# Kernel optimization log

Measured on AMD Instinct MI355X. Metric: run time of the kernel, lower is better.

The kernel has to match this reference:

```python
import jax, jax.numpy as jnp
import numpy as np

ANGLE_SCALE = 100.0
DIST_SCALE = 100.0
DIST_BOUNDARY = 0.0
HID = 128
N_HIDDEN = 2  # output_layer
EPS = 1e-08


def _mlp(x, w0, b0, ws, bs):
    # Linear, then N_HIDDEN x (ReLU, Linear)
    h = x @ w0 + b0
    for i in range(ws.shape[0]):
        h = jax.nn.relu(h) @ ws[i] + bs[i]
    return h


def _capsule_endpoints(x):
    # x: [..., 9] -> A, B endpoints of capsule segment, radius r
    c, s = jnp.cos(x[..., 3:4] * ANGLE_SCALE), jnp.sin(x[..., 3:4] * ANGLE_SCALE)
    half = x[..., 2:3] / 2
    ctr = x[..., 0:2]
    off = jnp.concatenate([half * c, half * s], axis=-1)
    return ctr - off, ctr + off, x[..., 4:5]


def _pt_seg_dist(P, A, AB, AB_sq):
    t = jnp.clip(((P - A) * AB).sum(-1, keepdims=True) / AB_sq, 0.0, 1.0)
    Q = A + t * AB
    return jnp.linalg.norm(P - Q, axis=-1, keepdims=True)


def _dist_to_capsule(init_e, query_e):
    A1, B1, r1 = _capsule_endpoints(init_e)
    A2, B2, r2 = _capsule_endpoints(query_e)
    A1B1, A2B2 = B1 - A1, B2 - A2
    s1 = (A1B1 ** 2).sum(-1, keepdims=True) + EPS
    s2 = (A2B2 ** 2).sum(-1, keepdims=True) + EPS
    d = jnp.minimum(
        jnp.minimum(_pt_seg_dist(A2, A1, A1B1, s1), _pt_seg_dist(B2, A1, A1B1, s1)),
        jnp.minimum(_pt_seg_dist(A1, A2, A2B2, s2), _pt_seg_dist(B1, A2, A2B2, s2)),
    )
    return d - r1 - r2


def setup_inputs() -> dict:
    key = jax.random.key(0)
    ks = jax.random.split(key, 32)
    B, O, T = 64, 64, 64
    f = lambda k, shp, scale=1.0: jax.random.normal(k, shp, dtype=jnp.float32) * scale
    inp = {
        'init_x': f(ks[0], (B, O, 9)),
        'query_x': f(ks[1], (B, T, 9)),
        'init_v': f(ks[2], (B, O, 2)),
        'query_v': f(ks[3], (B, T, 2)),
        'init_angular_v': f(ks[4], (B, O, 1)),
        'query_angular_v': f(ks[5], (B, T, 1)),
        'trunk_w0': f(ks[6], (9, HID), 0.3), 'trunk_b0': f(ks[7], (HID,), 0.1),
        'trunk_ws': f(ks[8], (N_HIDDEN, HID, HID), 0.08), 'trunk_bs': f(ks[9], (N_HIDDEN, HID), 0.1),
        'branch_w0': f(ks[10], (5, HID), 0.3), 'branch_b0': f(ks[11], (HID,), 0.1),
        'branch_ws': f(ks[12], (N_HIDDEN, HID, HID), 0.08), 'branch_bs': f(ks[13], (N_HIDDEN, HID), 0.1),
        'out_w': f(ks[14], (HID, 3), 0.08), 'out_b': f(ks[15], (3,), 0.1),
        'spring_w0': f(ks[16], (1, HID), 0.3), 'spring_b0': f(ks[17], (HID,), 0.1),
        'spring_w1': f(ks[18], (HID, 1), 0.08), 'spring_b1': f(ks[19], (1,), 0.1),
        'joint_w0': f(ks[20], (15, HID), 0.3), 'joint_b0': f(ks[21], (HID,), 0.1),
        'joint_w1': f(ks[22], (HID, 2), 0.08), 'joint_b1': f(ks[23], (2,), 0.1),
    }
    return inp


def reference(init_x, query_x, init_v, query_v, init_angular_v, query_angular_v,
              trunk_w0, trunk_b0, trunk_ws, trunk_bs,
              branch_w0, branch_b0, branch_ws, branch_bs,
              out_w, out_b, spring_w0, spring_b0, spring_w1, spring_b1,
              joint_w0, joint_b0, joint_w1, joint_b1):
    B, O, _ = init_x.shape
    T = query_x.shape[1]
    # pairwise broadcast: init along obj axis (dim1), query along target axis (dim2)
    init_e = jnp.broadcast_to(init_x[:, :, None, :], (B, O, T, 9))
    query_e = jnp.broadcast_to(query_x[:, None, :, :], (B, O, T, 9))
    rel = query_e[..., :2] - init_e[..., :2]
    query_e = jnp.concatenate([rel, query_e[..., 2:]], axis=-1)
    init_e = jnp.concatenate([jnp.zeros_like(rel), init_e[..., 2:]], axis=-1)
    qv = query_v[:, None, :, :] - init_v[:, :, None, :]           # [B,O,T,2]
    qav = query_angular_v[:, None, :, :] - init_angular_v[:, :, None, :]  # [B,O,T,1]
    iav = jnp.broadcast_to(init_angular_v[:, :, None, :], (B, O, T, 1))

    dist = _dist_to_capsule(init_e, query_e)
    dist_mask = (dist <= DIST_BOUNDARY).astype(jnp.float32)
    dist_input = dist * dist_mask * DIST_SCALE

    branch_in = init_e[..., :5]
    trunk_in = jnp.concatenate([query_e[..., :5], qv, qav, dist_input], axis=-1)
    branch_out = _mlp(branch_in, branch_w0, branch_b0, branch_ws, branch_bs)
    trunk_out = _mlp(trunk_in, trunk_w0, trunk_b0, trunk_ws, trunk_bs)
    force = (branch_out * trunk_out) @ out_w + out_b  # [B,O,T,3]

    # spring force
    have_spring = ((init_e[..., 8:9] == query_e[..., 8:9]) & (init_e[..., 8:9] > 0)).astype(jnp.float32)
    dvec = init_e[..., :2] - query_e[..., :2]
    length = jnp.linalg.norm(dvec, axis=-1, keepdims=True)
    dvec = dvec / (length + EPS)
    sf = jax.nn.relu(length @ spring_w0 + spring_b0) @ spring_w1 + spring_b1  # [B,O,T,1]
    sf = sf * dvec
    sf = jnp.concatenate([sf, jnp.zeros_like(sf[..., :1])], axis=-1) * have_spring

    # joint force (torch .long() truncates toward zero)
    i7, q7 = init_e[..., 7:8], query_e[..., 7:8]
    have_joint = ((jnp.trunc(i7) == jnp.trunc(q7)) & (i7 > 0)).astype(jnp.float32)
    joint_in = jnp.concatenate([init_e[..., :5], query_e[..., :5], qv, iav, qav, i7 - jnp.trunc(i7)], axis=-1)
    jf = jax.nn.relu(joint_in @ joint_w0 + joint_b0) @ joint_w1 + joint_b1  # [B,O,T,2]
    jf = jf * have_joint
    jf = jnp.concatenate([jf, jnp.zeros_like(jf[..., :1])], axis=-1)

    force = force * dist_mask + sf + jf
    return force
```

## Files before the change

kernel.cpp:

```cpp
#include <hip/hip_runtime.h>
#include <math.h>


typedef _Float16 h4v __attribute__((ext_vector_type(4)));
typedef _Float16 h8v __attribute__((ext_vector_type(8)));
typedef float    f4v __attribute__((ext_vector_type(4)));

#define AH 136

#define TW0_OFF 0
#define JW0_OFF 4096
#define TWS_OFF 8192
#define BW0_OFF 40960
#define BWS_OFF 45056
#define W_TOTAL 77824
#define BR_OFF_F (W_TOTAL/2)

#define H_ACTA 0
#define H_ACTB 8704
#define H_TINB 8704
#define H_JINB 10752
#define SMH_SIZE 17408

#define F_SCAL  0
#define SMF_SIZE 384

#define FRAG_BLOCKS 304
#define BR_BLOCKS   256

__global__ __launch_bounds__(256)
void prep_kernel(const float* __restrict__ tw0, const float* __restrict__ tws,
                 const float* __restrict__ jw0, const float* __restrict__ bw0,
                 const float* __restrict__ bws, const float* __restrict__ bb0,
                 const float* __restrict__ bbs, const float* __restrict__ init_x,
                 _Float16* __restrict__ wsH, float* __restrict__ brw)
{
    __shared__ float bsm[2*16*132];
    const int tid = threadIdx.x;

    if (blockIdx.x < FRAG_BLOCKS) {
        int idx = blockIdx.x * 256 + tid;
        if (idx >= W_TOTAL) return;
        const int j = idx & 7;
        const int lane = (idx >> 3) & 63;
        const int q = lane >> 4, r = lane & 15;
        _Float16 v;
        if (idx < JW0_OFF) {
            int mt = idx >> 9;
            int k = q*8 + j, m = mt*16 + r;
            v = (k < 9) ? (_Float16)tw0[k*128 + m] : (_Float16)0.f;
        } else if (idx < TWS_OFF) {
            int mt = (idx - JW0_OFF) >> 9;
            int k = q*8 + j, m = mt*16 + r;
            v = (k < 15) ? (_Float16)jw0[k*128 + m] : (_Float16)0.f;
        } else if (idx < BW0_OFF) {
            int e = idx - TWS_OFF;
            int ks = (e >> 9) & 3, mt = (e >> 11) & 7, l = e >> 14;
            int k = ks*32 + q*8 + j, m = mt*16 + r;
            v = (_Float16)tws[l*16384 + k*128 + m];
        } else if (idx < BWS_OFF) {
            int mt = (idx - BW0_OFF) >> 9;
            int k = q*8 + j, m = mt*16 + r;
            v = (k < 5) ? (_Float16)bw0[k*128 + m] : (_Float16)0.f;
        } else {
            int e = idx - BWS_OFF;
            int ks = (e >> 9) & 3, mt = (e >> 11) & 7, l = e >> 14;
            int k = ks*32 + q*8 + j, m = mt*16 + r;
            v = (_Float16)bws[l*16384 + k*128 + m];
        }
        wsH[idx] = v;
        return;
    }

    const int blk2 = blockIdx.x - FRAG_BLOCKS;
    const int row0 = blk2*16;
    const int lane = tid & 63, w = tid >> 6;
    const int q = lane >> 4, r = lane & 15;
    float* h0 = bsm;
    float* h1 = bsm + 16*132;

    for (int e = tid; e < 2048; e += 256) {
        const int rw = e >> 7, n = e & 127;
        const float* ixp = init_x + (row0 + rw)*9;
        float acc = bb0[n];
        acc = fmaf(ixp[2], bw0[2*128 + n], acc);
        acc = fmaf(ixp[3], bw0[3*128 + n], acc);
        acc = fmaf(ixp[4], bw0[4*128 + n], acc);
        h0[rw*132 + n] = acc;
    }
    __syncthreads();

    #pragma unroll
    for (int L = 0; L < 2; ++L) {
        const float* Wg = bws + L*16384;
        const float* bi = bbs + L*128;
        const float* in = (L == 0) ? h0 : h1;
        #pragma unroll
        for (int mi = 0; mi < 2; ++mi) {
            const int mt = w + mi*4;
            const int m0 = mt*16 + q*4;
            h8v af[4];
            #pragma unroll
            for (int ks = 0; ks < 4; ++ks)
                #pragma unroll
                for (int j = 0; j < 8; ++j)
                    af[ks][j] = (_Float16)Wg[(ks*32 + q*8 + j)*128 + mt*16 + r];
            f4v acc = *(const f4v*)&bi[m0];
            #pragma unroll
            for (int ks = 0; ks < 4; ++ks) {
                f4v x0 = *(const f4v*)&in[r*132 + ks*32 + q*8];
                f4v x1 = *(const f4v*)&in[r*132 + ks*32 + q*8 + 4];
                h8v bf;
                #pragma unroll
                for (int i = 0; i < 4; ++i) {
                    bf[i]   = (_Float16)fmaxf(x0[i], 0.f);
                    bf[4+i] = (_Float16)fmaxf(x1[i], 0.f);
                }
                acc = __builtin_amdgcn_mfma_f32_16x16x32_f16(af[ks], bf, acc, 0, 0, 0);
            }
            if (L == 0)
                *(f4v*)&h1[r*132 + m0] = acc;
            else
                *(f4v*)&brw[(row0 + r)*128 + m0] = acc;
        }
        __syncthreads();
    }
}

__device__ __forceinline__ void layerK32_rw(const h8v af[2],
        const float* __restrict__ bias, const _Float16* __restrict__ inB,
        _Float16* __restrict__ actOut, int lane, int w)
{
    const int q = lane >> 4, r = lane & 15;
    #pragma unroll
    for (int nt = 0; nt < 4; ++nt) {
        h8v bf = *(const h8v*)&inB[(nt*64 + lane)*8];
        #pragma unroll
        for (int mi = 0; mi < 2; ++mi) {
            f4v acc = *(const f4v*)&bias[(2*w + mi)*16 + q*4];
            acc = __builtin_amdgcn_mfma_f32_16x16x32_f16(af[mi], bf, acc, 0, 0, 0);
            h4v o;
            #pragma unroll
            for (int i = 0; i < 4; ++i) o[i] = (_Float16)fmaxf(acc[i], 0.f);
            *(h4v*)&actOut[(nt*16 + r)*AH + (2*w + mi)*16 + q*4] = o;
        }
    }
}

__device__ __forceinline__ void layerK128_rw(const h8v af[2][4],
        const float* __restrict__ bias, const _Float16* __restrict__ actIn,
        _Float16* __restrict__ actOut, int lane, int w)
{
    const int q = lane >> 4, r = lane & 15;
    #pragma unroll
    for (int nt = 0; nt < 4; ++nt) {
        h8v bf[4];
        #pragma unroll
        for (int ks = 0; ks < 4; ++ks)
            bf[ks] = *(const h8v*)&actIn[(nt*16 + r)*AH + ks*32 + q*8];
        #pragma unroll
        for (int mi = 0; mi < 2; ++mi) {
            f4v acc = *(const f4v*)&bias[(2*w + mi)*16 + q*4];
            #pragma unroll
            for (int ks = 0; ks < 4; ++ks)
                acc = __builtin_amdgcn_mfma_f32_16x16x32_f16(af[mi][ks], bf[ks], acc, 0, 0, 0);
            h4v o;
            #pragma unroll
            for (int i = 0; i < 4; ++i) o[i] = (_Float16)fmaxf(acc[i], 0.f);
            *(h4v*)&actOut[(nt*16 + r)*AH + (2*w + mi)*16 + q*4] = o;
        }
    }
}

__device__ __forceinline__ void layerK128_regs_rw(const h8v af[2][4],
        const float* __restrict__ bias, const _Float16* __restrict__ actIn,
        f4v accT[2][4], int lane, int w)
{
    const int q = lane >> 4, r = lane & 15;
    #pragma unroll
    for (int nt = 0; nt < 4; ++nt) {
        h8v bf[4];
        #pragma unroll
        for (int ks = 0; ks < 4; ++ks)
            bf[ks] = *(const h8v*)&actIn[(nt*16 + r)*AH + ks*32 + q*8];
        #pragma unroll
        for (int mi = 0; mi < 2; ++mi) {
            f4v acc = *(const f4v*)&bias[(2*w + mi)*16 + q*4];
            #pragma unroll
            for (int ks = 0; ks < 4; ++ks)
                acc = __builtin_amdgcn_mfma_f32_16x16x32_f16(af[mi][ks], bf[ks], acc, 0, 0, 0);
            accT[mi][nt] = acc;
        }
    }
}

__global__ __launch_bounds__(256, 3)
void ff_kernel(const float* __restrict__ init_x,  const float* __restrict__ query_x,
               const float* __restrict__ init_v,  const float* __restrict__ query_v,
               const float* __restrict__ init_av, const float* __restrict__ query_av,
               const float* __restrict__ tb0, const float* __restrict__ tbs,
               const float* __restrict__ out_w, const float* __restrict__ out_b,
               const float* __restrict__ sw0, const float* __restrict__ sb0,
               const float* __restrict__ sw1, const float* __restrict__ sb1,
               const float* __restrict__ jb0,
               const float* __restrict__ jw1, const float* __restrict__ jb1,
               const _Float16* __restrict__ wsH, const float* __restrict__ brw,
               float* __restrict__ out)
{
    __shared__ __align__(16) _Float16 smh[SMH_SIZE];
    __shared__ float smf[SMF_SIZE];
    float* const fred = (float*)smh;
    const int tid = threadIdx.x;
    const int bid = blockIdx.x;
    const int o  = bid & 63;
    const int b  = bid >> 6;
    const int lane = tid & 63, w = tid >> 6;
    const int q = lane >> 4, r = lane & 15;
    const float* ix = init_x + (b*64 + o)*9;

    h8v afT0[2], afJ0[2], afT1[2][4], afT2[2][4];
    f4v br[2];
    #pragma unroll
    for (int mi = 0; mi < 2; ++mi) {
        const int mtg = 2*w + mi;
        afT0[mi] = *(const h8v*)&wsH[TW0_OFF + (mtg*64 + lane)*8];
        afJ0[mi] = *(const h8v*)&wsH[JW0_OFF + (mtg*64 + lane)*8];
        #pragma unroll
        for (int ks = 0; ks < 4; ++ks) {
            afT1[mi][ks] = *(const h8v*)&wsH[TWS_OFF + ((mtg*4 + ks)*64 + lane)*8];
            afT2[mi][ks] = *(const h8v*)&wsH[TWS_OFF + 16384 + ((mtg*4 + ks)*64 + lane)*8];
        }
        br[mi] = *(const f4v*)&brw[bid*128 + mtg*16 + q*4];
    }

    {
        const int tq = w*16 + r;
        const float* qx = query_x + (b*64 + tq)*9;
        const float ix0 = ix[0], ix1 = ix[1], ix2 = ix[2], ix3 = ix[3], ix4 = ix[4];
        const float ix7 = ix[7], ix8 = ix[8];
        const float qx0 = qx[0], qx1 = qx[1], qx2 = qx[2], qx3 = qx[3], qx4 = qx[4];
        const float qx7 = qx[7], qx8 = qx[8];
        const float rel0 = qx0 - ix0, rel1 = qx1 - ix1;

        float s1v, c1v; sincosf(ix3 * 100.f, &s1v, &c1v);
        float s2v, c2v; sincosf(qx3 * 100.f, &s2v, &c2v);
        const float h1 = ix2 * 0.5f, h2 = qx2 * 0.5f;
        const float o1x = h1*c1v, o1y = h1*s1v;
        const float o2x = h2*c2v, o2y = h2*s2v;
        const float A1x = -o1x, A1y = -o1y;
        const float A2x = rel0 - o2x, A2y = rel1 - o2y;
        const float B2x = rel0 + o2x, B2y = rel1 + o2y;
        const float ab1x = 2.f*o1x, ab1y = 2.f*o1y;
        const float ab2x = 2.f*o2x, ab2y = 2.f*o2y;
        const float s1sq = ab1x*ab1x + ab1y*ab1y + 1e-8f;
        const float s2sq = ab2x*ab2x + ab2y*ab2y + 1e-8f;

        float Px, Py, Ax, Ay, ABx, ABy, ss;
        if (q < 2) {
            Ax = A1x; Ay = A1y; ABx = ab1x; ABy = ab1y; ss = s1sq;
            Px = (q == 0) ? A2x : B2x;  Py = (q == 0) ? A2y : B2y;
        } else {
            Ax = A2x; Ay = A2y; ABx = ab2x; ABy = ab2y; ss = s2sq;
            Px = (q == 2) ? A1x : o1x;  Py = (q == 2) ? A1y : o1y;
        }
        float t = ((Px - Ax)*ABx + (Py - Ay)*ABy) / ss;
        t = fminf(fmaxf(t, 0.f), 1.f);
        const float dx = Px - (Ax + t*ABx);
        const float dy = Py - (Ay + t*ABy);
        float dq = sqrtf(dx*dx + dy*dy);
        dq = fminf(dq, __shfl_xor(dq, 16));
        dq = fminf(dq, __shfl_xor(dq, 32));

        if (q == 0) {
            const float dist = dq - ix4 - qx4;
            const float mask = (dist <= 0.f) ? 1.f : 0.f;
            const float dinp = dist * mask * 100.f;
            const float qv0 = query_v[(b*64+tq)*2+0] - init_v[(b*64+o)*2+0];
            const float qv1 = query_v[(b*64+tq)*2+1] - init_v[(b*64+o)*2+1];
            const float iav = init_av[b*64+o];
            const float qav = query_av[b*64+tq] - iav;

            const int fb = w*512 + r*8;
            h8v t0, t1 = {}, z = {};
            t0[0]=(_Float16)rel0; t0[1]=(_Float16)rel1; t0[2]=(_Float16)qx2;
            t0[3]=(_Float16)qx3;  t0[4]=(_Float16)qx4;  t0[5]=(_Float16)qv0;
            t0[6]=(_Float16)qv1;  t0[7]=(_Float16)qav;
            t1[0]=(_Float16)dinp;
            *(h8v*)&smh[H_TINB + fb]       = t0;
            *(h8v*)&smh[H_TINB + fb + 128] = t1;
            *(h8v*)&smh[H_TINB + fb + 256] = z;
            *(h8v*)&smh[H_TINB + fb + 384] = z;
            h8v j0, j1 = {};
            j0[0]=(_Float16)0.f;  j0[1]=(_Float16)0.f;  j0[2]=(_Float16)ix2;
            j0[3]=(_Float16)ix3;  j0[4]=(_Float16)ix4;  j0[5]=(_Float16)rel0;
            j0[6]=(_Float16)rel1; j0[7]=(_Float16)qx2;
            j1[0]=(_Float16)qx3;  j1[1]=(_Float16)qx4;  j1[2]=(_Float16)qv0;
            j1[3]=(_Float16)qv1;  j1[4]=(_Float16)iav;  j1[5]=(_Float16)qav;
            j1[6]=(_Float16)(ix7 - truncf(ix7));
            *(h8v*)&smh[H_JINB + fb]       = j0;
            *(h8v*)&smh[H_JINB + fb + 128] = j1;
            *(h8v*)&smh[H_JINB + fb + 256] = z;
            *(h8v*)&smh[H_JINB + fb + 384] = z;

            const float len = sqrtf(rel0*rel0 + rel1*rel1);
            const float inv = 1.f / (len + 1e-8f);
            smf[F_SCAL +       tq] = mask;
            smf[F_SCAL +  64 + tq] = len;
            smf[F_SCAL + 128 + tq] = -rel0 * inv;
            smf[F_SCAL + 192 + tq] = -rel1 * inv;
            smf[F_SCAL + 256 + tq] = ((ix8 == qx8) && (ix8 > 0.f)) ? 1.f : 0.f;
            smf[F_SCAL + 320 + tq] = ((truncf(ix7) == truncf(qx7)) && (ix7 > 0.f)) ? 1.f : 0.f;
        }
    }
    __syncthreads();

    float jf0[4] = {0,0,0,0}, jf1[4] = {0,0,0,0};
    layerK32_rw(afT0, tb0, smh + H_TINB, smh + H_ACTA, lane, w);
    {
        f4v bv[2], jwa[2], jwb[2];
        #pragma unroll
        for (int mi = 0; mi < 2; ++mi) {
            const int m0 = (2*w + mi)*16 + q*4;
            bv[mi]  = *(const f4v*)&jb0[m0];
            jwa[mi] = *(const f4v*)&jw1[m0*2];
            jwb[mi] = *(const f4v*)&jw1[m0*2 + 4];
        }
        #pragma unroll
        for (int nt = 0; nt < 4; ++nt) {
            h8v bf = *(const h8v*)&smh[H_JINB + (nt*64 + lane)*8];
            #pragma unroll
            for (int mi = 0; mi < 2; ++mi) {
                f4v a = bv[mi];
                a = __builtin_amdgcn_mfma_f32_16x16x32_f16(afJ0[mi], bf, a, 0, 0, 0);
                float jw[8] = {jwa[mi][0], jwa[mi][1], jwa[mi][2], jwa[mi][3],
                               jwb[mi][0], jwb[mi][1], jwb[mi][2], jwb[mi][3]};
                #pragma unroll
                for (int i = 0; i < 4; ++i) {
                    const float jh = fmaxf(a[i], 0.f);
                    jf0[nt] = fmaf(jh, jw[i*2+0], jf0[nt]);
                    jf1[nt] = fmaf(jh, jw[i*2+1], jf1[nt]);
                }
            }
        }
    }
    __syncthreads();

    layerK128_rw(afT1, tbs, smh + H_ACTA, smh + H_ACTB, lane, w);
    __syncthreads();

    f4v accT[2][4];
    layerK128_regs_rw(afT2, tbs + 128, smh + H_ACTB, accT, lane, w);

    float f0[4] = {0,0,0,0}, f1[4] = {0,0,0,0}, f2[4] = {0,0,0,0};
    float sp[4] = {0,0,0,0};

    #pragma unroll
    for (int mi = 0; mi < 2; ++mi) {
        const int m0 = (2*w + mi)*16 + q*4;
        f4v oa = *(const f4v*)&out_w[m0*3];
        f4v ob = *(const f4v*)&out_w[m0*3 + 4];
        f4v oc = *(const f4v*)&out_w[m0*3 + 8];
        float ow[12] = {oa[0],oa[1],oa[2],oa[3], ob[0],ob[1],ob[2],ob[3],
                        oc[0],oc[1],oc[2],oc[3]};
        #pragma unroll
        for (int nt = 0; nt < 4; ++nt)
            #pragma unroll
            for (int i = 0; i < 4; ++i) {
                const float prod = accT[mi][nt][i] * br[mi][i];
                f0[nt] = fmaf(prod, ow[i*3+0], f0[nt]);
                f1[nt] = fmaf(prod, ow[i*3+1], f1[nt]);
                f2[nt] = fmaf(prod, ow[i*3+2], f2[nt]);
            }
    }
    {
        float lenv[4];
        #pragma unroll
        for (int nt = 0; nt < 4; ++nt) lenv[nt] = smf[F_SCAL + 64 + nt*16 + r];
        #pragma unroll
        for (int mi = 0; mi < 2; ++mi) {
            const int m0 = (2*w + mi)*16 + q*4;
            f4v w0 = *(const f4v*)&sw0[m0];
            f4v b0 = *(const f4v*)&sb0[m0];
            f4v w1 = *(const f4v*)&sw1[m0];
            #pragma unroll
            for (int i = 0; i < 4; ++i)
                #pragma unroll
                for (int nt = 0; nt < 4; ++nt) {
                    const float sv = fmaxf(fmaf(lenv[nt], w0[i], b0[i]), 0.f);
                    sp[nt] = fmaf(sv, w1[i], sp[nt]);
                }
        }
    }
    #pragma unroll
    for (int nt = 0; nt < 4; ++nt) {
        float v[6] = {f0[nt], f1[nt], f2[nt], jf0[nt], jf1[nt], sp[nt]};
        #pragma unroll
        for (int k = 0; k < 6; ++k) {
            v[k] += __shfl_xor(v[k], 16);
            v[k] += __shfl_xor(v[k], 32);
        }
        if (lane < 16) {
            float* rd = &fred[((nt*16 + r)*4 + w)*6];
            rd[0]=v[0]; rd[1]=v[1]; rd[2]=v[2]; rd[3]=v[3]; rd[4]=v[4]; rd[5]=v[5];
        }
    }
    __syncthreads();

    if (tid < 64) {
        const int t = tid;
        float s0=0.f, s1=0.f, s2=0.f, s3=0.f, s4=0.f, s5=0.f;
        #pragma unroll
        for (int ww = 0; ww < 4; ++ww) {
            const float* rd = &fred[(t*4 + ww)*6];
            s0 += rd[0]; s1 += rd[1]; s2 += rd[2];
            s3 += rd[3]; s4 += rd[4]; s5 += rd[5];
        }
        const float mask = smf[F_SCAL + t];
        const float dvx  = smf[F_SCAL + 128 + t];
        const float dvy  = smf[F_SCAL + 192 + t];
        const float hs   = smf[F_SCAL + 256 + t];
        const float hj   = smf[F_SCAL + 320 + t];
        const float sf = (s5 + sb1[0]) * hs;
        const float j0 = (s3 + jb1[0]) * hj;
        const float j1 = (s4 + jb1[1]) * hj;
        float* op = out + (((b*64 + o)*64) + t)*3;
        op[0] = (s0 + out_b[0])*mask + sf*dvx + j0;
        op[1] = (s1 + out_b[1])*mask + sf*dvy + j1;
        op[2] = (s2 + out_b[2])*mask;
    }
}

extern "C" void kernel_launch(void* const* d_in, const int* in_sizes, int n_in,
                              void* d_out, int out_size, void* d_ws, size_t ws_size,
                              hipStream_t stream) {
    (void)in_sizes; (void)n_in; (void)out_size; (void)ws_size;
    _Float16* wsH = (_Float16*)d_ws;
    float* brw = (float*)d_ws + BR_OFF_F;

    prep_kernel<<<dim3(FRAG_BLOCKS + BR_BLOCKS), dim3(256), 0, stream>>>(
        (const float*)d_in[6],
        (const float*)d_in[8],
        (const float*)d_in[20],
        (const float*)d_in[10],
        (const float*)d_in[12],
        (const float*)d_in[11],
        (const float*)d_in[13],
        (const float*)d_in[0],
        wsH, brw);
    ff_kernel<<<dim3(64*64), dim3(256), 0, stream>>>(
        (const float*)d_in[0],  (const float*)d_in[1],  (const float*)d_in[2],
        (const float*)d_in[3],  (const float*)d_in[4],  (const float*)d_in[5],
        (const float*)d_in[7],  (const float*)d_in[9],
        (const float*)d_in[14], (const float*)d_in[15],
        (const float*)d_in[16], (const float*)d_in[17],
        (const float*)d_in[18], (const float*)d_in[19],
        (const float*)d_in[21],
        (const float*)d_in[22], (const float*)d_in[23],
        wsH, brw, (float*)d_out);
}
```

Measured before the change: 155.4 us.

## Split MLP output tiles across eight waves per block instead of four

Doubles the block size to 512 threads so each wave owns a single 16-row output tile of every layer, halving the per-thread weight fragments held in registers. Later-layer weight fragments are now loaded just before use instead of all up front, and the capsule-distance prep and cross-wave reduction are remapped for eight waves. The aim is lower register pressure and more resident waves to hide MFMA and LDS latency, at the cost of a larger cross-wave reduction and more threads per barrier.

```diff
diff --git a/kernel.cpp b/kernel.cpp
--- a/kernel.cpp
+++ b/kernel.cpp
@@ -127,29 +127,26 @@
     }
 }
 
-__device__ __forceinline__ void layerK32_rw(const h8v af[2],
+__device__ __forceinline__ void layerK32_rw(const h8v af,
         const float* __restrict__ bias, const _Float16* __restrict__ inB,
-        _Float16* __restrict__ actOut, int lane, int w)
+        _Float16* __restrict__ actOut, int lane, int mtg)
 {
     const int q = lane >> 4, r = lane & 15;
     #pragma unroll
     for (int nt = 0; nt < 4; ++nt) {
         h8v bf = *(const h8v*)&inB[(nt*64 + lane)*8];
-        #pragma unroll
-        for (int mi = 0; mi < 2; ++mi) {
-            f4v acc = *(const f4v*)&bias[(2*w + mi)*16 + q*4];
-            acc = __builtin_amdgcn_mfma_f32_16x16x32_f16(af[mi], bf, acc, 0, 0, 0);
-            h4v o;
-            #pragma unroll
-            for (int i = 0; i < 4; ++i) o[i] = (_Float16)fmaxf(acc[i], 0.f);
-            *(h4v*)&actOut[(nt*16 + r)*AH + (2*w + mi)*16 + q*4] = o;
-        }
-    }
-}
-
-__device__ __forceinline__ void layerK128_rw(const h8v af[2][4],
+        f4v acc = *(const f4v*)&bias[mtg*16 + q*4];
+        acc = __builtin_amdgcn_mfma_f32_16x16x32_f16(af, bf, acc, 0, 0, 0);
+        h4v o;
+        #pragma unroll
+        for (int i = 0; i < 4; ++i) o[i] = (_Float16)fmaxf(acc[i], 0.f);
+        *(h4v*)&actOut[(nt*16 + r)*AH + mtg*16 + q*4] = o;
+    }
+}
+
+__device__ __forceinline__ void layerK128_rw(const h8v af[4],
         const float* __restrict__ bias, const _Float16* __restrict__ actIn,
-        _Float16* __restrict__ actOut, int lane, int w)
+        _Float16* __restrict__ actOut, int lane, int mtg)
 {
     const int q = lane >> 4, r = lane & 15;
     #pragma unroll
@@ -158,23 +155,20 @@
         #pragma unroll
         for (int ks = 0; ks < 4; ++ks)
             bf[ks] = *(const h8v*)&actIn[(nt*16 + r)*AH + ks*32 + q*8];
-        #pragma unroll
-        for (int mi = 0; mi < 2; ++mi) {
-            f4v acc = *(const f4v*)&bias[(2*w + mi)*16 + q*4];
-            #pragma unroll
-            for (int ks = 0; ks < 4; ++ks)
-                acc = __builtin_amdgcn_mfma_f32_16x16x32_f16(af[mi][ks], bf[ks], acc, 0, 0, 0);
-            h4v o;
-            #pragma unroll
-            for (int i = 0; i < 4; ++i) o[i] = (_Float16)fmaxf(acc[i], 0.f);
-            *(h4v*)&actOut[(nt*16 + r)*AH + (2*w + mi)*16 + q*4] = o;
-        }
-    }
-}
-
-__device__ __forceinline__ void layerK128_regs_rw(const h8v af[2][4],
+        f4v acc = *(const f4v*)&bias[mtg*16 + q*4];
+        #pragma unroll
+        for (int ks = 0; ks < 4; ++ks)
+            acc = __builtin_amdgcn_mfma_f32_16x16x32_f16(af[ks], bf[ks], acc, 0, 0, 0);
+        h4v o;
+        #pragma unroll
+        for (int i = 0; i < 4; ++i) o[i] = (_Float16)fmaxf(acc[i], 0.f);
+        *(h4v*)&actOut[(nt*16 + r)*AH + mtg*16 + q*4] = o;
+    }
+}
+
+__device__ __forceinline__ void layerK128_regs_rw(const h8v af[4],
         const float* __restrict__ bias, const _Float16* __restrict__ actIn,
-        f4v accT[2][4], int lane, int w)
+        f4v accT[4], int lane, int mtg)
 {
     const int q = lane >> 4, r = lane & 15;
     #pragma unroll
@@ -183,18 +177,15 @@
         #pragma unroll
         for (int ks = 0; ks < 4; ++ks)
             bf[ks] = *(const h8v*)&actIn[(nt*16 + r)*AH + ks*32 + q*8];
-        #pragma unroll
-        for (int mi = 0; mi < 2; ++mi) {
-            f4v acc = *(const f4v*)&bias[(2*w + mi)*16 + q*4];
-            #pragma unroll
-            for (int ks = 0; ks < 4; ++ks)
-                acc = __builtin_amdgcn_mfma_f32_16x16x32_f16(af[mi][ks], bf[ks], acc, 0, 0, 0);
-            accT[mi][nt] = acc;
-        }
-    }
-}
-
-__global__ __launch_bounds__(256, 3)
+        f4v acc = *(const f4v*)&bias[mtg*16 + q*4];
+        #pragma unroll
+        for (int ks = 0; ks < 4; ++ks)
+            acc = __builtin_amdgcn_mfma_f32_16x16x32_f16(af[ks], bf[ks], acc, 0, 0, 0);
+        accT[nt] = acc;
+    }
+}
+
+__global__ __launch_bounds__(512, 6)
 void ff_kernel(const float* __restrict__ init_x,  const float* __restrict__ query_x,
                const float* __restrict__ init_v,  const float* __restrict__ query_v,
                const float* __restrict__ init_av, const float* __restrict__ query_av,
@@ -218,23 +209,14 @@
     const int q = lane >> 4, r = lane & 15;
     const float* ix = init_x + (b*64 + o)*9;
 
-    h8v afT0[2], afJ0[2], afT1[2][4], afT2[2][4];
-    f4v br[2];
-    #pragma unroll
-    for (int mi = 0; mi < 2; ++mi) {
-        const int mtg = 2*w + mi;
-        afT0[mi] = *(const h8v*)&wsH[TW0_OFF + (mtg*64 + lane)*8];
-        afJ0[mi] = *(const h8v*)&wsH[JW0_OFF + (mtg*64 + lane)*8];
-        #pragma unroll
-        for (int ks = 0; ks < 4; ++ks) {
-            afT1[mi][ks] = *(const h8v*)&wsH[TWS_OFF + ((mtg*4 + ks)*64 + lane)*8];
-            afT2[mi][ks] = *(const h8v*)&wsH[TWS_OFF + 16384 + ((mtg*4 + ks)*64 + lane)*8];
-        }
-        br[mi] = *(const f4v*)&brw[bid*128 + mtg*16 + q*4];
-    }
+    h8v afT0 = *(const h8v*)&wsH[TW0_OFF + (w*64 + lane)*8];
+    h8v afJ0 = *(const h8v*)&wsH[JW0_OFF + (w*64 + lane)*8];
+    f4v br   = *(const f4v*)&brw[bid*128 + w*16 + q*4];
 
     {
-        const int tq = w*16 + r;
+        const int rq   = lane & 7;
+        const int cand = (lane >> 3) & 3;
+        const int tq   = w*8 + rq;
         const float* qx = query_x + (b*64 + tq)*9;
         const float ix0 = ix[0], ix1 = ix[1], ix2 = ix[2], ix3 = ix[3], ix4 = ix[4];
         const float ix7 = ix[7], ix8 = ix[8];
@@ -256,22 +238,22 @@
         const float s2sq = ab2x*ab2x + ab2y*ab2y + 1e-8f;
 
         float Px, Py, Ax, Ay, ABx, ABy, ss;
-        if (q < 2) {
+        if (cand < 2) {
             Ax = A1x; Ay = A1y; ABx = ab1x; ABy = ab1y; ss = s1sq;
-            Px = (q == 0) ? A2x : B2x;  Py = (q == 0) ? A2y : B2y;
+            Px = (cand == 0) ? A2x : B2x;  Py = (cand == 0) ? A2y : B2y;
         } else {
             Ax = A2x; Ay = A2y; ABx = ab2x; ABy = ab2y; ss = s2sq;
-            Px = (q == 2) ? A1x : o1x;  Py = (q == 2) ? A1y : o1y;
+            Px = (cand == 2) ? A1x : o1x;  Py = (cand == 2) ? A1y : o1y;
         }
         float t = ((Px - Ax)*ABx + (Py - Ay)*ABy) / ss;
         t = fminf(fmaxf(t, 0.f), 1.f);
         const float dx = Px - (Ax + t*ABx);
         const float dy = Py - (Ay + t*ABy);
         float dq = sqrtf(dx*dx + dy*dy);
+        dq = fminf(dq, __shfl_xor(dq, 8));
         dq = fminf(dq, __shfl_xor(dq, 16));
-        dq = fminf(dq, __shfl_xor(dq, 32));
-
-        if (q == 0) {
+
+        if ((lane & 56) == 0) {
             const float dist = dq - ix4 - qx4;
             const float mask = (dist <= 0.f) ? 1.f : 0.f;
             const float dinp = dist * mask * 100.f;
@@ -280,7 +262,7 @@
             const float iav = init_av[b*64+o];
             const float qav = query_av[b*64+tq] - iav;
 
-            const int fb = w*512 + r*8;
+            const int fb = (tq >> 4)*512 + (tq & 15)*8;
             h8v t0, t1 = {}, z = {};
             t0[0]=(_Float16)rel0; t0[1]=(_Float16)rel1; t0[2]=(_Float16)qx2;
             t0[3]=(_Float16)qx3;  t0[4]=(_Float16)qx4;  t0[5]=(_Float16)qv0;
@@ -314,49 +296,51 @@
     }
     __syncthreads();
 
+    h8v afT1[4];
+    #pragma unroll
+    for (int ks = 0; ks < 4; ++ks)
+        afT1[ks] = *(const h8v*)&wsH[TWS_OFF + ((w*4 + ks)*64 + lane)*8];
+
     float jf0[4] = {0,0,0,0}, jf1[4] = {0,0,0,0};
     layerK32_rw(afT0, tb0, smh + H_TINB, smh + H_ACTA, lane, w);
     {
-        f4v bv[2], jwa[2], jwb[2];
-        #pragma unroll
-        for (int mi = 0; mi < 2; ++mi) {
-            const int m0 = (2*w + mi)*16 + q*4;
-            bv[mi]  = *(const f4v*)&jb0[m0];
-            jwa[mi] = *(const f4v*)&jw1[m0*2];
-            jwb[mi] = *(const f4v*)&jw1[m0*2 + 4];
-        }
+        const int m0 = w*16 + q*4;
+        f4v bv  = *(const f4v*)&jb0[m0];
+        f4v jwa = *(const f4v*)&jw1[m0*2];
+        f4v jwb = *(const f4v*)&jw1[m0*2 + 4];
         #pragma unroll
         for (int nt = 0; nt < 4; ++nt) {
             h8v bf = *(const h8v*)&smh[H_JINB + (nt*64 + lane)*8];
+            f4v a = bv;
+            a = __builtin_amdgcn_mfma_f32_16x16x32_f16(afJ0, bf, a, 0, 0, 0);
+            float jw[8] = {jwa[0], jwa[1], jwa[2], jwa[3],
+                           jwb[0], jwb[1], jwb[2], jwb[3]};
             #pragma unroll
-            for (int mi = 0; mi < 2; ++mi) {
-                f4v a = bv[mi];
-                a = __builtin_amdgcn_mfma_f32_16x16x32_f16(afJ0[mi], bf, a, 0, 0, 0);
-                float jw[8] = {jwa[mi][0], jwa[mi][1], jwa[mi][2], jwa[mi][3],
-                               jwb[mi][0], jwb[mi][1], jwb[mi][2], jwb[mi][3]};
-                #pragma unroll
-                for (int i = 0; i < 4; ++i) {
-                    const float jh = fmaxf(a[i], 0.f);
-                    jf0[nt] = fmaf(jh, jw[i*2+0], jf0[nt]);
-                    jf1[nt] = fmaf(jh, jw[i*2+1], jf1[nt]);
-                }
+            for (int i = 0; i < 4; ++i) {
+                const float jh = fmaxf(a[i], 0.f);
+                jf0[nt] = fmaf(jh, jw[i*2+0], jf0[nt]);
+                jf1[nt] = fmaf(jh, jw[i*2+1], jf1[nt]);
             }
         }
     }
     __syncthreads();
+
+    h8v afT2[4];
+    #pragma unroll
+    for (int ks = 0; ks < 4; ++ks)
+        afT2[ks] = *(const h8v*)&wsH[TWS_OFF + 16384 + ((w*4 + ks)*64 + lane)*8];
 
     layerK128_rw(afT1, tbs, smh + H_ACTA, smh + H_ACTB, lane, w);
     __syncthreads();
 
-    f4v accT[2][4];
+    f4v accT[4];
     layerK128_regs_rw(afT2, tbs + 128, smh + H_ACTB, accT, lane, w);
 
     float f0[4] = {0,0,0,0}, f1[4] = {0,0,0,0}, f2[4] = {0,0,0,0};
     float sp[4] = {0,0,0,0};
 
-    #pragma unroll
-    for (int mi = 0; mi < 2; ++mi) {
-        const int m0 = (2*w + mi)*16 + q*4;
+    {
+        const int m0 = w*16 + q*4;
         f4v oa = *(const f4v*)&out_w[m0*3];
         f4v ob = *(const f4v*)&out_w[m0*3 + 4];
         f4v oc = *(const f4v*)&out_w[m0*3 + 8];
@@ -366,7 +350,7 @@
         for (int nt = 0; nt < 4; ++nt)
             #pragma unroll
             for (int i = 0; i < 4; ++i) {
-                const float prod = accT[mi][nt][i] * br[mi][i];
+                const float prod = accT[nt][i] * br[i];
                 f0[nt] = fmaf(prod, ow[i*3+0], f0[nt]);
                 f1[nt] = fmaf(prod, ow[i*3+1], f1[nt]);
                 f2[nt] = fmaf(prod, ow[i*3+2], f2[nt]);
@@ -376,20 +360,17 @@
         float lenv[4];
         #pragma unroll
         for (int nt = 0; nt < 4; ++nt) lenv[nt] = smf[F_SCAL + 64 + nt*16 + r];
-        #pragma unroll
-        for (int mi = 0; mi < 2; ++mi) {
-            const int m0 = (2*w + mi)*16 + q*4;
-            f4v w0 = *(const f4v*)&sw0[m0];
-            f4v b0 = *(const f4v*)&sb0[m0];
-            f4v w1 = *(const f4v*)&sw1[m0];
+        const int m0 = w*16 + q*4;
+        f4v w0v = *(const f4v*)&sw0[m0];
+        f4v b0v = *(const f4v*)&sb0[m0];
+        f4v w1v = *(const f4v*)&sw1[m0];
+        #pragma unroll
+        for (int i = 0; i < 4; ++i)
             #pragma unroll
-            for (int i = 0; i < 4; ++i)
-                #pragma unroll
-                for (int nt = 0; nt < 4; ++nt) {
-                    const float sv = fmaxf(fmaf(lenv[nt], w0[i], b0[i]), 0.f);
-                    sp[nt] = fmaf(sv, w1[i], sp[nt]);
-                }
-        }
+            for (int nt = 0; nt < 4; ++nt) {
+                const float sv = fmaxf(fmaf(lenv[nt], w0v[i], b0v[i]), 0.f);
+                sp[nt] = fmaf(sv, w1v[i], sp[nt]);
+            }
     }
     #pragma unroll
     for (int nt = 0; nt < 4; ++nt) {
@@ -400,7 +381,7 @@
             v[k] += __shfl_xor(v[k], 32);
         }
         if (lane < 16) {
-            float* rd = &fred[((nt*16 + r)*4 + w)*6];
+            float* rd = &fred[(w*64 + nt*16 + r)*7];
             rd[0]=v[0]; rd[1]=v[1]; rd[2]=v[2]; rd[3]=v[3]; rd[4]=v[4]; rd[5]=v[5];
         }
     }
@@ -410,8 +391,8 @@
         const int t = tid;
         float s0=0.f, s1=0.f, s2=0.f, s3=0.f, s4=0.f, s5=0.f;
         #pragma unroll
-        for (int ww = 0; ww < 4; ++ww) {
-            const float* rd = &fred[(t*4 + ww)*6];
+        for (int ww = 0; ww < 8; ++ww) {
+            const float* rd = &fred[(ww*64 + t)*7];
             s0 += rd[0]; s1 += rd[1]; s2 += rd[2];
             s3 += rd[3]; s4 += rd[4]; s5 += rd[5];
         }
@@ -447,7 +428,7 @@
         (const float*)d_in[13],
         (const float*)d_in[0],
         wsH, brw);
-    ff_kernel<<<dim3(64*64), dim3(256), 0, stream>>>(
+    ff_kernel<<<dim3(64*64), dim3(512), 0, stream>>>(
         (const float*)d_in[0],  (const float*)d_in[1],  (const float*)d_in[2],
         (const float*)d_in[3],  (const float*)d_in[4],  (const float*)d_in[5],
         (const float*)d_in[7],  (const float*)d_in[9],
```

Measured after the change: 172.0 us. +10.7%, slower.
